# Performance work log

Hardware: AMD Instinct MI355X
Metric: run time of the kernel (lower is better)

The kernel has to match this reference:

```python
import jax, jax.numpy as jnp
import numpy as np

D = 128
H = 128  # scorer hidden

def setup_inputs() -> dict:
    key = jax.random.key(0)
    ks = jax.random.split(key, 8)
    B, T = 4096, 200
    transformer_out = jax.random.normal(ks[0], (B, T, D), dtype=jnp.float32)
    candidate = jax.random.normal(ks[1], (B, D), dtype=jnp.float32)
    mask = jax.random.randint(ks[2], (B, T), 0, 2).astype(jnp.bool_)
    # scorer params: Linear(3D,H) -> PReLU -> Linear(H,1)
    lim1 = 1.0 / np.sqrt(3 * D)
    W1 = jax.random.uniform(ks[3], (3 * D, H), minval=-lim1, maxval=lim1, dtype=jnp.float32)
    b1 = jax.random.uniform(ks[4], (H,), minval=-lim1, maxval=lim1, dtype=jnp.float32)
    a = jnp.array(0.25, dtype=jnp.float32)  # PReLU default init
    lim2 = 1.0 / np.sqrt(H)
    W2 = jax.random.uniform(ks[5], (H, 1), minval=-lim2, maxval=lim2, dtype=jnp.float32)
    b2 = jax.random.uniform(ks[6], (1,), minval=-lim2, maxval=lim2, dtype=jnp.float32)
    return {"transformer_out": transformer_out, "candidate": candidate, "mask": mask,
            "W1": W1, "b1": b1, "a": a, "W2": W2, "b2": b2}

def reference(transformer_out, candidate, mask, W1, b1, a, W2, b2):
    # transformer_out: [B,T,D], candidate: [B,D]
    cand_exp = jnp.broadcast_to(candidate[:, None, :], transformer_out.shape)  # [B,T,D]
    att_input = jnp.concatenate([transformer_out, cand_exp, transformer_out * cand_exp], axis=-1)  # [B,T,3D]
    h = att_input @ W1 + b1                       # [B,T,H]
    h = jnp.where(h >= 0, h, a * h)               # PReLU (single shared alpha)
    scores = (h @ W2 + b2)[..., 0]                # [B,T]
    scores = jnp.where(mask, scores, -jnp.inf)
    weights = jax.nn.softmax(scores, axis=-1)     # [B,T]
    return jnp.einsum('bt,btd->bd', weights, transformer_out)  # [B,D]
```

## Files before the change

kernel.cpp:

```cpp
#include <hip/hip_runtime.h>
#include <hip/hip_bf16.h>

typedef __attribute__((ext_vector_type(8))) short short8;
typedef __attribute__((ext_vector_type(4))) float f32x4;

#define B_T 200
#define B_D 128

static __device__ __forceinline__ short f2bf(float f) {
  unsigned u = __builtin_bit_cast(unsigned, f);
  u += 0x7fffu + ((u >> 16) & 1u);
  return (short)(u >> 16);
}
static __device__ __forceinline__ float bf2f(short s) {
  unsigned u = ((unsigned)(unsigned short)s) << 16;
  return __builtin_bit_cast(float, u);
}
static __device__ __forceinline__ short8 cvt8(f32x4 a, f32x4 b) {
  short8 t;
  t[0] = f2bf(a[0]); t[1] = f2bf(a[1]); t[2] = f2bf(a[2]); t[3] = f2bf(a[3]);
  t[4] = f2bf(b[0]); t[5] = f2bf(b[1]); t[6] = f2bf(b[2]); t[7] = f2bf(b[3]);
  return t;
}

__global__ __launch_bounds__(256) void ta_prep_w(const float* __restrict__ W1,
                                                 short* __restrict__ wfrag) {
  const int o = blockIdx.x * 256 + threadIdx.x;
  const int j = o & 127, k0 = (o >> 7) * 8;
  short8 ta, tc;
  #pragma unroll
  for (int e = 0; e < 8; ++e) {
    ta[e] = f2bf(W1[(size_t)(k0 + e) * B_D + j]);
    tc[e] = f2bf(W1[(size_t)(256 + k0 + e) * B_D + j]);
  }
  *(short8*)&wfrag[o * 8] = ta;
  *(short8*)&wfrag[16384 + o * 8] = tc;
}

__global__ __launch_bounds__(256) void ta_prep_beta(const float* __restrict__ cand,
                                                    const float* __restrict__ W1,
                                                    const float* __restrict__ b1,
                                                    float* __restrict__ beta, int B) {
  __shared__ float w1b[B_D][B_D];
  const int tid = threadIdx.x;
  #pragma unroll
  for (int i = 0; i < 16; ++i) {
    int v = i * 256 + tid;
    ((f32x4*)w1b)[v] = ((const f32x4*)(W1 + 128 * B_D))[v];
  }
  __syncthreads();
  const int j = tid & 127, which = tid >> 7;
  const int b0 = blockIdx.x * 8;
  #pragma unroll
  for (int bi = 0; bi < 4; ++bi) {
    int b = b0 + bi * 2 + which;
    if (b < B) {
      const float* cb = cand + (size_t)b * B_D;
      float s0 = b1[j], s1 = 0.f, s2 = 0.f, s3 = 0.f;
      #pragma unroll 8
      for (int k = 0; k < 128; k += 4) {
        s0 = fmaf(cb[k    ], w1b[k    ][j], s0);
        s1 = fmaf(cb[k + 1], w1b[k + 1][j], s1);
        s2 = fmaf(cb[k + 2], w1b[k + 2][j], s2);
        s3 = fmaf(cb[k + 3], w1b[k + 3][j], s3);
      }
      beta[(size_t)b * B_D + j] = (s0 + s1) + (s2 + s3);
    }
  }
}

__global__ __launch_bounds__(256, 4)
void ta_fused(const float* __restrict__ x,
              const float* __restrict__ cand,
              const void*  __restrict__ maskp,
              const float* __restrict__ W1,
              const float* __restrict__ b1,
              const float* __restrict__ ap,
              const float* __restrict__ W2,
              const short* __restrict__ wfrag,
              const float* __restrict__ beta,
              int use_ws,
              float* __restrict__ out)
{
  __shared__ __align__(16) short wbt[B_D * B_D];
  __shared__ float bpart[2][B_D];
  __shared__ float w2_lds[B_D];
  __shared__ float scores[208];
  __shared__ float red[8];
  float (*part)[B_D] = (float (*)[B_D])wbt;

  const int b    = blockIdx.x;
  const int tid  = threadIdx.x;
  const int lane = tid & 63;
  const int wv   = tid >> 6;
  const int l15  = lane & 15;
  const int g    = lane >> 4;

  int flag1b;
  {
    const unsigned char* mb = (const unsigned char*)maskp;
    unsigned long long v8 = *(const unsigned long long*)(mb + lane * 8);
    flag1b = __any((v8 & 0xFFFFFF00FFFFFF00ull) != 0ull);
  }
  bool mk = false;
  if (tid < B_T) {
    if (flag1b) mk = ((const unsigned char*)maskp)[(size_t)b * B_T + tid] != 0;
    else        mk = ((const int*)maskp)[(size_t)b * B_T + tid] != 0;
  }

  if (tid < B_D) w2_lds[tid] = W2[tid];

  const float* cb = cand + (size_t)b * B_D;
  if (use_ws) {
    #pragma unroll 2
    for (int it = 0; it < 8; ++it) {
      const int o = it * 256 + tid;
      const int k0 = (o >> 7) * 8;
      short8 wa = *(const short8*)&wfrag[o * 8];
      short8 wc = *(const short8*)&wfrag[16384 + o * 8];
      short8 t;
      #pragma unroll
      for (int e = 0; e < 8; ++e)
        t[e] = f2bf(fmaf(cb[k0 + e], bf2f(wc[e]), bf2f(wa[e])));
      *(short8*)&wbt[o * 8] = t;
    }
  } else {
    const int j = tid & 127, h = tid >> 7;
    #pragma unroll 2
    for (int it = 0; it < 8; ++it) {
      const int ko = it * 2 + h, k0 = ko * 8;
      short8 t;
      #pragma unroll
      for (int e = 0; e < 8; ++e) {
        float c  = cb[k0 + e];
        float wa = W1[(size_t)(k0 + e) * B_D + j];
        float wc = W1[(size_t)(256 + k0 + e) * B_D + j];
        t[e] = f2bf(fmaf(c, wc, wa));
      }
      *(short8*)&wbt[(ko * B_D + j) * 8] = t;
    }
    float s0 = (h == 0) ? b1[j] : 0.f, s1 = 0.f, s2 = 0.f, s3 = 0.f;
    const float* w1b = W1 + (size_t)(B_D + h * 64) * B_D + j;
    #pragma unroll 8
    for (int k = 0; k < 64; k += 4) {
      s0 = fmaf(cb[h * 64 + k    ], w1b[(size_t)(k    ) * B_D], s0);
      s1 = fmaf(cb[h * 64 + k + 1], w1b[(size_t)(k + 1) * B_D], s1);
      s2 = fmaf(cb[h * 64 + k + 2], w1b[(size_t)(k + 2) * B_D], s2);
      s3 = fmaf(cb[h * 64 + k + 3], w1b[(size_t)(k + 3) * B_D], s3);
    }
    bpart[h][j] = (s0 + s1) + (s2 + s3);
  }
  __syncthreads();

  float betaL[8], w2L[8];
  #pragma unroll
  for (int nt = 0; nt < 8; ++nt) {
    int col = nt * 16 + l15;
    betaL[nt] = use_ws ? beta[(size_t)b * B_D + col] : (bpart[0][col] + bpart[1][col]);
    w2L[nt]   = w2_lds[col];
  }
  const float alpha = ap[0];

#define TILE_SCORE(MT) do {                                                   \
    int row = (MT) * 16 + l15; if (row > B_T - 1) row = B_T - 1;              \
    const float* xr = x + ((size_t)b * B_T + row) * B_D + g * 8;              \
    f32x4 p0 = *(const f32x4*)(xr +  0), p1 = *(const f32x4*)(xr +   4);      \
    f32x4 p2 = *(const f32x4*)(xr + 32), p3 = *(const f32x4*)(xr +  36);      \
    f32x4 p4 = *(const f32x4*)(xr + 64), p5 = *(const f32x4*)(xr +  68);      \
    f32x4 p6 = *(const f32x4*)(xr + 96), p7 = *(const f32x4*)(xr + 100);      \
    short8 a0 = cvt8(p0, p1), a1 = cvt8(p2, p3);                              \
    short8 a2 = cvt8(p4, p5), a3 = cvt8(p6, p7);                              \
    float sc[4] = {0.f, 0.f, 0.f, 0.f};                                       \
    _Pragma("unroll")                                                         \
    for (int nt = 0; nt < 8; ++nt) {                                          \
      f32x4 acc = {0.f, 0.f, 0.f, 0.f};                                       \
      const short8* wp = (const short8*)wbt + g * B_D + nt * 16 + l15;        \
      acc = __builtin_amdgcn_mfma_f32_16x16x32_bf16(a0, wp[0],    acc, 0,0,0);\
      acc = __builtin_amdgcn_mfma_f32_16x16x32_bf16(a1, wp[512],  acc, 0,0,0);\
      acc = __builtin_amdgcn_mfma_f32_16x16x32_bf16(a2, wp[1024], acc, 0,0,0);\
      acc = __builtin_amdgcn_mfma_f32_16x16x32_bf16(a3, wp[1536], acc, 0,0,0);\
      _Pragma("unroll")                                                       \
      for (int r = 0; r < 4; ++r) {                                           \
        float h = acc[r] + betaL[nt];                                         \
        float p = (h >= 0.f) ? h : alpha * h;                                 \
        sc[r] += p * w2L[nt];                                                 \
      }                                                                       \
    }                                                                         \
    _Pragma("unroll")                                                         \
    for (int r = 0; r < 4; ++r) {                                             \
      float v = sc[r];                                                        \
      v += __shfl_xor(v, 1, 16); v += __shfl_xor(v, 2, 16);                   \
      v += __shfl_xor(v, 4, 16); v += __shfl_xor(v, 8, 16);                   \
      if (l15 == 0) scores[(MT) * 16 + g * 4 + r] = v;                        \
    }                                                                         \
  } while (0)

  TILE_SCORE(wv);
  TILE_SCORE(4 + wv);
  TILE_SCORE(8 + wv);
  if (wv == 0) TILE_SCORE(12);
#undef TILE_SCORE
  __syncthreads();

  {
    float s = (tid < B_T && mk) ? scores[tid] : -INFINITY;
    float v = s;
    #pragma unroll
    for (int m = 32; m >= 1; m >>= 1) v = fmaxf(v, __shfl_xor(v, m, 64));
    if (lane == 0) red[wv] = v;
    __syncthreads();
    float mx = fmaxf(fmaxf(red[0], red[1]), fmaxf(red[2], red[3]));
    float e = mk ? __expf(s - mx) : 0.f;
    float sv = e;
    #pragma unroll
    for (int m = 32; m >= 1; m >>= 1) sv += __shfl_xor(sv, m, 64);
    if (lane == 0) red[4 + wv] = sv;
    if (tid < 208) scores[tid] = e;
    __syncthreads();
  }

  {
    const int d4 = (tid & 31) << 2;
    const int p  = tid >> 5;
    const float* xc = x + ((size_t)b * B_T + p * 25) * B_D + d4;
    f32x4 acc = {0.f, 0.f, 0.f, 0.f};
    #pragma unroll 5
    for (int t = 0; t < 25; ++t) {
      f32x4 xv = *(const f32x4*)(xc + (size_t)t * B_D);
      float w = scores[p * 25 + t];
      acc[0] = fmaf(w, xv[0], acc[0]);
      acc[1] = fmaf(w, xv[1], acc[1]);
      acc[2] = fmaf(w, xv[2], acc[2]);
      acc[3] = fmaf(w, xv[3], acc[3]);
    }
    *(f32x4*)&part[p][d4] = acc;
  }
  __syncthreads();
  if (tid < B_D) {
    float Z = (red[4] + red[5]) + (red[6] + red[7]);
    float s = 0.f;
    #pragma unroll
    for (int p = 0; p < 8; ++p) s += part[p][tid];
    out[(size_t)b * B_D + tid] = s / Z;
  }
}

extern "C" void kernel_launch(void* const* d_in, const int* in_sizes, int n_in,
                              void* d_out, int out_size, void* d_ws, size_t ws_size,
                              hipStream_t stream) {
  const float* x    = (const float*)d_in[0];
  const float* cand = (const float*)d_in[1];
  const void*  mask = d_in[2];
  const float* W1   = (const float*)d_in[3];
  const float* b1   = (const float*)d_in[4];
  const float* a    = (const float*)d_in[5];
  const float* W2   = (const float*)d_in[6];
  float* out = (float*)d_out;
  const int B = in_sizes[1] / B_D;

  short* wfrag = (short*)d_ws;
  float* beta  = (float*)((char*)d_ws + 65536);
  const size_t need = 65536 + (size_t)B * B_D * sizeof(float);
  const int use_ws = (ws_size >= need) ? 1 : 0;

  if (use_ws) {
    ta_prep_w<<<8, 256, 0, stream>>>(W1, wfrag);
    ta_prep_beta<<<(B + 7) / 8, 256, 0, stream>>>(cand, W1, b1, beta, B);
  }
  ta_fused<<<B, 256, 0, stream>>>(x, cand, mask, W1, b1, a, W2,
                                  wfrag, beta, use_ws, out);
}
```

Measured before the change: 152.1 us.

## Fuse softmax and weighted sum into score tiles with online softmax

Replaces the separate score-write, block softmax, and second pass over x with an online-softmax accumulation. Each wave reuses the x rows already loaded in registers for the MFMA to accumulate exp-weighted outputs, rescaling when the running max grows. This removes the second global read of x and two block barriers. In exchange it holds 32 extra fp32 accumulators per thread, which raises register pressure at launch bound 4, and adds shuffles and rescaling work per tile.

```diff
diff --git a/kernel.cpp b/kernel.cpp
--- a/kernel.cpp
+++ b/kernel.cpp
@@ -84,8 +84,6 @@
 {
   __shared__ __align__(16) short wbt[B_D * B_D];
   __shared__ float bpart[2][B_D];
-  __shared__ float w2_lds[B_D];
-  __shared__ float scores[208];
   __shared__ float red[8];
   float (*part)[B_D] = (float (*)[B_D])wbt;
 
@@ -102,13 +100,15 @@
     unsigned long long v8 = *(const unsigned long long*)(mb + lane * 8);
     flag1b = __any((v8 & 0xFFFFFF00FFFFFF00ull) != 0ull);
   }
-  bool mk = false;
-  if (tid < B_T) {
-    if (flag1b) mk = ((const unsigned char*)maskp)[(size_t)b * B_T + tid] != 0;
-    else        mk = ((const int*)maskp)[(size_t)b * B_T + tid] != 0;
-  }
-
-  if (tid < B_D) w2_lds[tid] = W2[tid];
+  const unsigned char* mb8 = (const unsigned char*)maskp;
+  const int* mb32 = (const int*)maskp;
+  #define LDMK(ROW) (flag1b ? (mb8[(size_t)b * B_T + (ROW)] != 0) \
+                            : (mb32[(size_t)b * B_T + (ROW)] != 0))
+  const bool mk0 = LDMK(wv * 16 + l15);
+  const bool mk1 = LDMK((4 + wv) * 16 + l15);
+  const bool mk2 = LDMK((8 + wv) * 16 + l15);
+  const bool mk3 = (wv == 0) ? LDMK(192 + l15 < B_T ? 192 + l15 : B_T - 1) : false;
+  #undef LDMK
 
   const float* cb = cand + (size_t)b * B_D;
   if (use_ws) {
@@ -157,13 +157,20 @@
   for (int nt = 0; nt < 8; ++nt) {
     int col = nt * 16 + l15;
     betaL[nt] = use_ws ? beta[(size_t)b * B_D + col] : (bpart[0][col] + bpart[1][col]);
-    w2L[nt]   = w2_lds[col];
+    w2L[nt]   = W2[col];
   }
   const float alpha = ap[0];
 
-#define TILE_SCORE(MT) do {                                                   \
-    int row = (MT) * 16 + l15; if (row > B_T - 1) row = B_T - 1;              \
-    const float* xr = x + ((size_t)b * B_T + row) * B_D + g * 8;              \
+  float m = -INFINITY, Z = 0.f;
+  float O[32];
+  #pragma unroll
+  for (int i = 0; i < 32; ++i) O[i] = 0.f;
+
+#define TILE_ONLINE(MT, MKV) do {                                             \
+    const int rowi = (MT) * 16 + l15;                                         \
+    const bool rv = rowi < B_T;                                               \
+    const int rowc = rv ? rowi : (B_T - 1);                                   \
+    const float* xr = x + ((size_t)b * B_T + rowc) * B_D + g * 8;             \
     f32x4 p0 = *(const f32x4*)(xr +  0), p1 = *(const f32x4*)(xr +   4);      \
     f32x4 p2 = *(const f32x4*)(xr + 32), p3 = *(const f32x4*)(xr +  36);      \
     f32x4 p4 = *(const f32x4*)(xr + 64), p5 = *(const f32x4*)(xr +  68);      \
@@ -188,60 +195,68 @@
     }                                                                         \
     _Pragma("unroll")                                                         \
     for (int r = 0; r < 4; ++r) {                                             \
-      float v = sc[r];                                                        \
-      v += __shfl_xor(v, 1, 16); v += __shfl_xor(v, 2, 16);                   \
-      v += __shfl_xor(v, 4, 16); v += __shfl_xor(v, 8, 16);                   \
-      if (l15 == 0) scores[(MT) * 16 + g * 4 + r] = v;                        \
+      sc[r] += __shfl_xor(sc[r], 1, 16); sc[r] += __shfl_xor(sc[r], 2, 16);   \
+      sc[r] += __shfl_xor(sc[r], 4, 16); sc[r] += __shfl_xor(sc[r], 8, 16);   \
+    }                                                                         \
+    float tmax = fmaxf(fmaxf(sc[0], sc[1]), fmaxf(sc[2], sc[3]));             \
+    tmax = fmaxf(tmax, __shfl_xor(tmax, 16, 64));                             \
+    tmax = fmaxf(tmax, __shfl_xor(tmax, 32, 64));                             \
+    if (tmax > m) {                                         \
+      float rs = __expf(m - tmax); m = tmax; Z *= rs;                         \
+      _Pragma("unroll") for (int i2 = 0; i2 < 32; ++i2) O[i2] *= rs;          \
+    }                                                                         \
+    float vsel = sc[0];                                                       \
+    vsel = ((l15 & 3) == 1) ? sc[1] : vsel;                                   \
+    vsel = ((l15 & 3) == 2) ? sc[2] : vsel;                                   \
+    vsel = ((l15 & 3) == 3) ? sc[3] : vsel;                                   \
+    float srow = __shfl(vsel, (l15 >> 2) * 16 + l15, 64);                     \
+    float ew = (rv && (MKV)) ? __expf(srow - m) : 0.f;                        \
+    float ts = ew;                                                            \
+    ts += __shfl_xor(ts, 1, 16); ts += __shfl_xor(ts, 2, 16);                 \
+    ts += __shfl_xor(ts, 4, 16); ts += __shfl_xor(ts, 8, 16);                 \
+    Z += ts;                                                                  \
+    _Pragma("unroll")                                                         \
+    for (int e2 = 0; e2 < 4; ++e2) {                                          \
+      O[ 0 + e2] = fmaf(ew, p0[e2], O[ 0 + e2]);                              \
+      O[ 4 + e2] = fmaf(ew, p1[e2], O[ 4 + e2]);                              \
+      O[ 8 + e2] = fmaf(ew, p2[e2], O[ 8 + e2]);                              \
+      O[12 + e2] = fmaf(ew, p3[e2], O[12 + e2]);                              \
+      O[16 + e2] = fmaf(ew, p4[e2], O[16 + e2]);                              \
+      O[20 + e2] = fmaf(ew, p5[e2], O[20 + e2]);                              \
+      O[24 + e2] = fmaf(ew, p6[e2], O[24 + e2]);                              \
+      O[28 + e2] = fmaf(ew, p7[e2], O[28 + e2]);                              \
     }                                                                         \
   } while (0)
 
-  TILE_SCORE(wv);
-  TILE_SCORE(4 + wv);
-  TILE_SCORE(8 + wv);
-  if (wv == 0) TILE_SCORE(12);
-#undef TILE_SCORE
-  __syncthreads();
-
-  {
-    float s = (tid < B_T && mk) ? scores[tid] : -INFINITY;
-    float v = s;
+  TILE_ONLINE(wv, mk0);
+  TILE_ONLINE(4 + wv, mk1);
+  TILE_ONLINE(8 + wv, mk2);
+  if (wv == 0) TILE_ONLINE(12, mk3);
+#undef TILE_ONLINE
+
+  if (lane == 0) { red[wv] = m; red[4 + wv] = Z; }
+  __syncthreads();
+  float mg = fmaxf(fmaxf(red[0], red[1]), fmaxf(red[2], red[3]));
+  float Zg = red[4] * __expf(red[0] - mg) + red[5] * __expf(red[1] - mg)
+           + red[6] * __expf(red[2] - mg) + red[7] * __expf(red[3] - mg);
+  const float fac = __expf(m - mg) / Zg;
+
+  #pragma unroll
+  for (int i = 0; i < 32; ++i) {
+    float v = O[i] * fac;
+    v += __shfl_xor(v, 1, 16); v += __shfl_xor(v, 2, 16);
+    v += __shfl_xor(v, 4, 16); v += __shfl_xor(v, 8, 16);
+    O[i] = v;
+  }
+  if (l15 == 0) {
     #pragma unroll
-    for (int m = 32; m >= 1; m >>= 1) v = fmaxf(v, __shfl_xor(v, m, 64));
-    if (lane == 0) red[wv] = v;
-    __syncthreads();
-    float mx = fmaxf(fmaxf(red[0], red[1]), fmaxf(red[2], red[3]));
-    float e = mk ? __expf(s - mx) : 0.f;
-    float sv = e;
-    #pragma unroll
-    for (int m = 32; m >= 1; m >>= 1) sv += __shfl_xor(sv, m, 64);
-    if (lane == 0) red[4 + wv] = sv;
-    if (tid < 208) scores[tid] = e;
-    __syncthreads();
-  }
-
-  {
-    const int d4 = (tid & 31) << 2;
-    const int p  = tid >> 5;
-    const float* xc = x + ((size_t)b * B_T + p * 25) * B_D + d4;
-    f32x4 acc = {0.f, 0.f, 0.f, 0.f};
-    #pragma unroll 5
-    for (int t = 0; t < 25; ++t) {
-      f32x4 xv = *(const f32x4*)(xc + (size_t)t * B_D);
-      float w = scores[p * 25 + t];
-      acc[0] = fmaf(w, xv[0], acc[0]);
-      acc[1] = fmaf(w, xv[1], acc[1]);
-      acc[2] = fmaf(w, xv[2], acc[2]);
-      acc[3] = fmaf(w, xv[3], acc[3]);
-    }
-    *(f32x4*)&part[p][d4] = acc;
+    for (int i = 0; i < 32; ++i)
+      part[wv][(i >> 3) * 32 + g * 8 + (i & 7)] = O[i];
   }
   __syncthreads();
   if (tid < B_D) {
-    float Z = (red[4] + red[5]) + (red[6] + red[7]);
-    float s = 0.f;
-    #pragma unroll
-    for (int p = 0; p < 8; ++p) s += part[p][tid];
-    out[(size_t)b * B_D + tid] = s / Z;
+    out[(size_t)b * B_D + tid] =
+        (part[0][tid] + part[1][tid]) + (part[2][tid] + part[3][tid]);
   }
 }
 
```

New measurement: 246.1 us. 1.62x slower.
